# Optimization experiments

Measured on AMD Instinct MI355X. Metric: run time of the kernel, lower is better.

## Reference

```python
import jax, jax.numpy as jnp
import numpy as np

B, T, D_IN, H, D = 4, 4096, 1024, 16, 64


def setup_inputs() -> dict:
    key = jax.random.key(0)
    k1, k2, k3 = jax.random.split(key, 3)
    inputs = jax.random.normal(k1, (B, T, D_IN), dtype=jnp.float32)
    kv_kernel = jax.random.normal(k2, (D_IN, H, D, 2), dtype=jnp.float32) * (1.0 / np.sqrt(D_IN))
    q_kernel = jax.random.normal(k3, (H, D), dtype=jnp.float32) * (1.0 / np.sqrt(D))
    return {"inputs": inputs, "kv_kernel": kv_kernel, "q_kernel": q_kernel}


def _associate(a, b):
    # Online-softmax combine on packed tuples [m(1), u(1), w(D)] along last axis.
    ma, ua, wa = a[..., :1], a[..., 1:2], a[..., 2:]
    mb, ub, wb = b[..., :1], b[..., 1:2], b[..., 2:]
    m = jnp.maximum(ma, mb)
    ea = jnp.exp(ma - m)
    eb = jnp.exp(mb - m)
    u = ua * ea + ub * eb
    w = wa * ea + wb * eb
    return jnp.concatenate([m, u, w], axis=-1)


def reference(inputs, kv_kernel, q_kernel):
    # inputs: (B,T,D_in); kv_kernel: (D_in,H,D,2); q_kernel: (H,D)
    kv = jnp.einsum('bti,ihdk->bthdk', inputs, kv_kernel)
    kv = jax.nn.relu(kv)  # activation; dropout disabled (inference)
    k = kv[..., 0]  # (B,T,H,D)
    v = kv[..., 1]  # (B,T,H,D)
    st = jnp.einsum('hd,bthd->bth', q_kernel, k)[..., None]  # (B,T,H,1)
    u_init = jnp.ones_like(st)  # exp(s - m) with m = s
    elems = jnp.concatenate([st, u_init, v], axis=-1)  # (B,T,H,D+2)
    o = jax.lax.associative_scan(_associate, elems, axis=1)
    c = o[..., 1:2]  # running denominator
    a = o[..., 2:]   # running numerator (B,T,H,D)
    h = a / c
    # concat_heads=False -> sum over heads
    return jnp.sum(h, axis=-2)  # (B,T,D)
```

## Files before the change

kernel.cpp:

```cpp
#include <hip/hip_runtime.h>
#include <hip/hip_bf16.h>
#include <math.h>

#define B_   4
#define T_   4096
#define DIN_ 1024
#define H_   16
#define D_   64
#define M_   (B_*T_)
#define N_   (H_*D_*2)
#define K_   DIN_
#define C_   64
#define CL_  (T_/C_)

typedef unsigned short u16;
typedef __attribute__((ext_vector_type(8))) short short8_t;
typedef __attribute__((ext_vector_type(4))) float float4_t;

__device__ __forceinline__ u16 f2bf(float f) {
  unsigned int x = __float_as_uint(f);
  x += 0x7fffu + ((x >> 16) & 1u);
  return (u16)(x >> 16);
}
__device__ __forceinline__ float bf2f(unsigned int u) {
  return __uint_as_float((u & 0xffffu) << 16);
}
__device__ __forceinline__ unsigned pk_bf16(float x, float y) {
  float2 f; f.x = x; f.y = y;
  union { __hip_bfloat162 h2; unsigned u; } c;
  c.h2 = __float22bfloat162_rn(f);
  return c.u;
}

__device__ __forceinline__ void g2l16(const u16* g, u16* l) {
  __builtin_amdgcn_global_load_lds(
      (const __attribute__((address_space(1))) void*)g,
      (__attribute__((address_space(3))) void*)l, 16, 0, 0);
}

__global__ __launch_bounds__(256)
void prep(const float* __restrict__ inputs, const float* __restrict__ kvk,
          u16* __restrict__ aB, u16* __restrict__ wBt) {
  __shared__ float tile[32][33];
  int bid = blockIdx.x;
  int tid = threadIdx.x;
  if (bid < 8192) {
    int i = bid * 256 + tid;
    const float4* src = (const float4*)inputs;
    float4 a = src[2*i], b = src[2*i+1];
    uint4 o;
    o.x = pk_bf16(a.x, a.y);
    o.y = pk_bf16(a.z, a.w);
    o.z = pk_bf16(b.x, b.y);
    o.w = pk_bf16(b.z, b.w);
    ((uint4*)aB)[i] = o;
  } else {
    int b2 = bid - 8192;
    int kb = (b2 & 31) * 32;
    int nb = (b2 >> 5) * 32;
    int r  = tid >> 3;
    int c4 = (tid & 7) * 4;
    float4 v = *(const float4*)&kvk[(size_t)(kb + r) * N_ + nb + c4];
    tile[r][c4+0] = v.x; tile[r][c4+1] = v.y; tile[r][c4+2] = v.z; tile[r][c4+3] = v.w;
    __syncthreads();
    uint2 o;
    o.x = pk_bf16(tile[c4+0][r], tile[c4+1][r]);
    o.y = pk_bf16(tile[c4+2][r], tile[c4+3][r]);
    *(uint2*)&wBt[(size_t)(nb + r) * K_ + kb + c4] = o;
  }
}


#define FENCE asm volatile("" ::: "memory")
#define KBAR do { FENCE; __builtin_amdgcn_s_barrier(); FENCE; } while (0)

#define READS(PAR) do { _Pragma("unroll") \
  for (int i_ = 0; i_ < 4; ++i_) \
    af[i_] = *(const short8_t*)&lds[(PAR)*8192 + aBase + i_*512]; \
  _Pragma("unroll") \
  for (int j_ = 0; j_ < 4; ++j_) \
    bfq[j_] = *(const short8_t*)&lds[(PAR)*8192 + bBase + j_*512]; \
} while (0)

#define MFMAS do { \
  __builtin_amdgcn_s_setprio(1); \
  _Pragma("unroll") for (int i_ = 0; i_ < 4; ++i_) \
  _Pragma("unroll") for (int j_ = 0; j_ < 4; ++j_) \
    acc[i_][j_] = __builtin_amdgcn_mfma_f32_16x16x32_bf16( \
        af[i_], bfq[j_], acc[i_][j_], 0, 0, 0); \
  __builtin_amdgcn_s_setprio(0); \
} while (0)

#define PHASE(PAR, PAR2, KT) do { \
  short8_t af[4], bfq[4]; \
  READS(PAR); \
  g2l16(gA + ((KT)+2)*32, lds +         (PAR2)*8192 + wv*512); \
  g2l16(gB + ((KT)+2)*32, lds + 24576 + (PAR2)*8192 + wv*512); \
  KBAR; \
  MFMAS; \
  asm volatile("s_waitcnt vmcnt(2)" ::: "memory"); \
  KBAR; \
} while (0)

__global__ __launch_bounds__(1024)
void gemm_kv(const u16* __restrict__ A, const u16* __restrict__ Bt,
             const float* __restrict__ q,
             float* __restrict__ pbuf, u16* __restrict__ vbuf,
             float* __restrict__ aggU, float* __restrict__ aggW) {
  extern __shared__ __align__(16) char smem[];
  u16* lds = (u16*)smem;

  const int tid  = threadIdx.x;
  const int wv   = tid >> 6;
  const int lane = tid & 63;
  const int quad = lane >> 4;
  const int l16  = lane & 15;
  const int wr2  = wv >> 2;
  const int wc2  = wv & 3;

  const int g  = blockIdx.x;
  const int wg = (g & 7) * 64 + (g >> 3);
  const int nt = wg & 7;
  const int mt = wg >> 3;
  const int bm = mt * 256;
  const int bn = nt * 256;

  const u16* gA = A  + (size_t)(bm + (tid >> 2)) * K_ + (((tid & 3) ^ ((tid >> 3) & 3)) * 8);
  const u16* gB = Bt + (size_t)(bn + (tid >> 2)) * K_ + (((tid & 3) ^ ((tid >> 3) & 3)) * 8);

  const int sg    = (quad ^ ((l16 >> 1) & 3)) * 8;
  const int aBase = wr2 * 2048 + l16 * 32 + sg;
  const int bBase = 24576 + wc2 * 2048 + l16 * 32 + sg;

  float4_t acc[4][4] = {};

  g2l16(gA,      lds +                 wv*512);
  g2l16(gB,      lds + 24576 +         wv*512);
  g2l16(gA + 32, lds +          8192 + wv*512);
  g2l16(gB + 32, lds + 24576 +  8192 + wv*512);
  asm volatile("s_waitcnt vmcnt(2)" ::: "memory");
  KBAR;

#pragma unroll 1
  for (int kq = 0; kq < 10; ++kq) {
    const int kt = kq * 3;
    PHASE(0, 2, kt + 0);
    PHASE(1, 0, kt + 1);
    PHASE(2, 1, kt + 2);
  }
  {
    short8_t af[4], bfq[4];
    READS(0);
    KBAR;
    MFMAS;
    asm volatile("s_waitcnt vmcnt(0)" ::: "memory");
    KBAR;
  }
  {
    short8_t af[4], bfq[4];
    READS(1);
    KBAR;
    MFMAS;
    KBAR;
  }

  u16*   vtile = (u16*)smem;
  float* sred  = (float*)(smem + 73728);
  float* pS    = (float*)(smem + 83968);

  const int nh   = wc2 >> 1;
  const int wc2p = wc2 & 1;
  const int hd   = l16 >> 1;

  float qv[4];
#pragma unroll
  for (int j = 0; j < 4; ++j)
    qv[j] = q[(nt*2 + nh)*64 + wc2p*32 + j*8 + hd];

#pragma unroll
  for (int i = 0; i < 4; ++i) {
#pragma unroll
    for (int r = 0; r < 4; ++r) {
      const int t = wr2*64 + i*16 + quad*4 + r;
      float x0 = fmaxf(acc[i][0][r], 0.f);
      float x1 = fmaxf(acc[i][1][r], 0.f);
      float x2 = fmaxf(acc[i][2][r], 0.f);
      float x3 = fmaxf(acc[i][3][r], 0.f);
      if (l16 & 1) {
        vtile[(nh*256 + t)*72 + wc2p*32 +  0 + hd] = f2bf(x0);
        vtile[(nh*256 + t)*72 + wc2p*32 +  8 + hd] = f2bf(x1);
        vtile[(nh*256 + t)*72 + wc2p*32 + 16 + hd] = f2bf(x2);
        vtile[(nh*256 + t)*72 + wc2p*32 + 24 + hd] = f2bf(x3);
      } else {
        float ps = qv[0]*x0 + qv[1]*x1 + qv[2]*x2 + qv[3]*x3;
        ps += __shfl_xor(ps, 2);
        ps += __shfl_xor(ps, 4);
        if ((l16 & 7) == 0)
          sred[(nh*256 + t)*5 + wc2p*2 + (l16 >> 3)] = ps;
      }
    }
  }
  __syncthreads();

  const int b  = mt >> 4;
  const int t0 = (mt & 15) * 256;
  if (tid < 512) {
    const int hh = tid >> 8;
    const int t  = tid & 255;
    const float* sr = &sred[(hh*256 + t)*5];
    float s = sr[0] + sr[1] + sr[2] + sr[3];
    float p = __expf(fminf(fmaxf(s, -60.f), 60.f));
    pS[hh*256 + t] = p;
    pbuf[(size_t)(b*H_ + nt*2 + hh) * T_ + t0 + t] = p;
    float u = p;
#pragma unroll
    for (int off = 32; off; off >>= 1) u += __shfl_down(u, off);
    if (lane == 0)
      aggU[(b*H_ + nt*2 + hh)*C_ + (mt & 15)*4 + ((tid >> 6) & 3)] = u;
  }
  __syncthreads();

  if (l16 & 1) {
    float Wv[4] = {};
#pragma unroll
    for (int i = 0; i < 4; ++i)
#pragma unroll
      for (int r = 0; r < 4; ++r) {
        const int t = wr2*64 + i*16 + quad*4 + r;
        const float p = pS[nh*256 + t];
        Wv[0] += p * fmaxf(acc[i][0][r], 0.f);
        Wv[1] += p * fmaxf(acc[i][1][r], 0.f);
        Wv[2] += p * fmaxf(acc[i][2][r], 0.f);
        Wv[3] += p * fmaxf(acc[i][3][r], 0.f);
      }
#pragma unroll
    for (int j = 0; j < 4; ++j) {
      float w = Wv[j];
      w += __shfl_xor(w, 16);
      w += __shfl_xor(w, 32);
      if (quad == 0) {
        const int blk = (b*H_ + nt*2 + nh)*C_ + (mt & 15)*4 + wr2;
        aggW[(size_t)blk * D_ + wc2p*32 + j*8 + hd] = w;
      }
    }
  }
  {
    const int d0 = (tid & 7) * 8;
#pragma unroll
    for (int k2 = 0; k2 < 4; ++k2) {
      const int row = (tid >> 3) + 128*k2;
      const int hh  = row >> 8;
      const int t   = row & 255;
      uint4 val = *(const uint4*)&vtile[(hh*256 + t)*72 + d0];
      *(uint4*)&vbuf[((size_t)(b*H_ + nt*2 + hh) * T_ + t0 + t) * D_ + d0] = val;
    }
  }
}

__global__ __launch_bounds__(1024)
void scan_pass3(const u16* __restrict__ vbuf, const float* __restrict__ pbuf,
                const float* __restrict__ aggU, const float* __restrict__ aggW,
                float* __restrict__ out) {
  __shared__ float pS[H_][CL_];
  __shared__ float wbuf[H_][8][D_ + 1];
  int bc = blockIdx.x;
  int b  = bc >> 6;
  int c  = bc & (C_ - 1);
  int tid  = threadIdx.x;
  int h    = tid >> 6;
  int lane = tid & 63;
  int bh   = b * H_ + h;
  int t0   = c * CL_;

  pS[h][lane] = pbuf[(size_t)bh * T_ + t0 + lane];

  float U = 0.f, W = 0.f;
  for (int j = 0; j < c; ++j) {
    int idx = bh * C_ + j;
    U += aggU[idx];
    W += aggW[(size_t)idx * D_ + lane];
  }
  __syncthreads();

  const u16* vp = vbuf + ((size_t)bh * T_ + t0) * D_ + lane;
  for (int gg = 0; gg < 8; ++gg) {
#pragma unroll
    for (int ii = 0; ii < 8; ++ii) {
      int i = gg * 8 + ii;
      float p = pS[h][i];
      float v = bf2f(vp[i * D_]);
      U += p;
      W += p * v;
      wbuf[h][ii][lane] = __fdividef(W, U);
    }
    __syncthreads();
    if (tid < 512) {
      int ii = tid >> 6, dd = tid & 63;
      float acc = 0.f;
#pragma unroll
      for (int hh = 0; hh < H_; ++hh) acc += wbuf[hh][ii][dd];
      out[((size_t)b * T_ + t0 + gg*8 + ii) * D_ + dd] = acc;
    }
    __syncthreads();
  }
}

extern "C" void kernel_launch(void* const* d_in, const int* in_sizes, int n_in,
                              void* d_out, int out_size, void* d_ws, size_t ws_size,
                              hipStream_t stream) {
  const float* inputs = (const float*)d_in[0];
  const float* kvk    = (const float*)d_in[1];
  const float* qk     = (const float*)d_in[2];
  float* out = (float*)d_out;
  char* ws = (char*)d_ws;

  u16*   aB   = (u16*)ws;
  u16*   wBt  = (u16*)(ws + 33554432);
  u16*   vb   = (u16*)(ws + 37748736);
  float* pb   = (float*)(ws + 71303168);
  float* aggU = (float*)(ws + 72351744);
  float* aggW = (float*)(ws + 72368128);

  prep<<<10240, 256, 0, stream>>>(inputs, kvk, aB, wBt);
  gemm_kv<<<512, 1024, 98304, stream>>>(aB, wBt, qk, pb, vb, aggU, aggW);
  scan_pass3<<<B_*C_, 1024, 0, stream>>>(vb, pb, aggU, aggW, out);
}
```

Baseline: 202.5 us.

## Switch KV GEMM to 32x32x16 MFMA with 4-stage K16 pipeline and register double-buffering

Replaces the 16x16x32 MFMA tiling with 32x32x16 bf16 MFMAs. The K loop now uses a 4-deep LDS ring of K=16 slices, and fragment loads are double-buffered in registers so LDS reads overlap the MFMAs, with one barrier per step instead of two. The epilogue is remapped to the 32x32 accumulator layout. The prep kernel's conversion loads are split into two coalesced halves. This trades more barriers per K (64 smaller steps) and an unswizzled LDS layout (possible bank conflicts) for fewer instructions per FLOP and better overlap.

```diff
diff --git a/kernel.cpp b/kernel.cpp
--- a/kernel.cpp
+++ b/kernel.cpp
@@ -15,7 +15,7 @@
 
 typedef unsigned short u16;
 typedef __attribute__((ext_vector_type(8))) short short8_t;
-typedef __attribute__((ext_vector_type(4))) float float4_t;
+typedef __attribute__((ext_vector_type(16))) float f32x16;
 
 __device__ __forceinline__ u16 f2bf(float f) {
   unsigned int x = __float_as_uint(f);
@@ -45,15 +45,14 @@
   int bid = blockIdx.x;
   int tid = threadIdx.x;
   if (bid < 8192) {
-    int i = bid * 256 + tid;
-    const float4* src = (const float4*)inputs;
-    float4 a = src[2*i], b = src[2*i+1];
-    uint4 o;
-    o.x = pk_bf16(a.x, a.y);
-    o.y = pk_bf16(a.z, a.w);
-    o.z = pk_bf16(b.x, b.y);
-    o.w = pk_bf16(b.z, b.w);
-    ((uint4*)aB)[i] = o;
+    int j = bid * 256 + tid;
+    const float4* s4 = (const float4*)inputs;
+    float4 a = s4[j];
+    float4 b = s4[j + 2097152];
+    uint2 oa; oa.x = pk_bf16(a.x, a.y); oa.y = pk_bf16(a.z, a.w);
+    uint2 ob; ob.x = pk_bf16(b.x, b.y); ob.y = pk_bf16(b.z, b.w);
+    ((uint2*)aB)[j]           = oa;
+    ((uint2*)aB)[j + 2097152] = ob;
   } else {
     int b2 = bid - 8192;
     int kb = (b2 & 31) * 32;
@@ -74,31 +73,29 @@
 #define FENCE asm volatile("" ::: "memory")
 #define KBAR do { FENCE; __builtin_amdgcn_s_barrier(); FENCE; } while (0)
 
-#define READS(PAR) do { _Pragma("unroll") \
-  for (int i_ = 0; i_ < 4; ++i_) \
-    af[i_] = *(const short8_t*)&lds[(PAR)*8192 + aBase + i_*512]; \
-  _Pragma("unroll") \
-  for (int j_ = 0; j_ < 4; ++j_) \
-    bfq[j_] = *(const short8_t*)&lds[(PAR)*8192 + bBase + j_*512]; \
+#define MFMA32(a,b,c) __builtin_amdgcn_mfma_f32_32x32x16_bf16(a,b,c,0,0,0)
+
+#define LOADS(PN, AF, BF) do { \
+  AF[0] = *(const short8_t*)&lds[(PN)*4096 + aOff      ]; \
+  AF[1] = *(const short8_t*)&lds[(PN)*4096 + aOff + 512]; \
+  BF[0] = *(const short8_t*)&lds[16384 + (PN)*4096 + bOff      ]; \
+  BF[1] = *(const short8_t*)&lds[16384 + (PN)*4096 + bOff + 512]; \
 } while (0)
 
-#define MFMAS do { \
+#define MMAS(AF, BF) do { \
   __builtin_amdgcn_s_setprio(1); \
-  _Pragma("unroll") for (int i_ = 0; i_ < 4; ++i_) \
-  _Pragma("unroll") for (int j_ = 0; j_ < 4; ++j_) \
-    acc[i_][j_] = __builtin_amdgcn_mfma_f32_16x16x32_bf16( \
-        af[i_], bfq[j_], acc[i_][j_], 0, 0, 0); \
+  acc[0][0] = MFMA32(AF[0], BF[0], acc[0][0]); \
+  acc[0][1] = MFMA32(AF[0], BF[1], acc[0][1]); \
+  acc[1][0] = MFMA32(AF[1], BF[0], acc[1][0]); \
+  acc[1][1] = MFMA32(AF[1], BF[1], acc[1][1]); \
   __builtin_amdgcn_s_setprio(0); \
 } while (0)
 
-#define PHASE(PAR, PAR2, KT) do { \
-  short8_t af[4], bfq[4]; \
-  READS(PAR); \
-  g2l16(gA + ((KT)+2)*32, lds +         (PAR2)*8192 + wv*512); \
-  g2l16(gB + ((KT)+2)*32, lds + 24576 + (PAR2)*8192 + wv*512); \
-  KBAR; \
-  MFMAS; \
-  asm volatile("s_waitcnt vmcnt(2)" ::: "memory"); \
+#define PHASE(KT, PN, PS, AFm, BFm, AFl, BFl) do { \
+  LOADS(PN, AFl, BFl); \
+  g2l16(gS + (size_t)((KT)+3)*16, lds + stBase + (PS)*4096); \
+  MMAS(AFm, BFm); \
+  asm volatile("s_waitcnt vmcnt(1)" ::: "memory"); \
   KBAR; \
 } while (0)
 
@@ -113,8 +110,8 @@
   const int tid  = threadIdx.x;
   const int wv   = tid >> 6;
   const int lane = tid & 63;
-  const int quad = lane >> 4;
-  const int l16  = lane & 15;
+  const int l31  = lane & 31;
+  const int hi   = lane >> 5;
   const int wr2  = wv >> 2;
   const int wc2  = wv & 3;
 
@@ -125,78 +122,86 @@
   const int bm = mt * 256;
   const int bn = nt * 256;
 
-  const u16* gA = A  + (size_t)(bm + (tid >> 2)) * K_ + (((tid & 3) ^ ((tid >> 3) & 3)) * 8);
-  const u16* gB = Bt + (size_t)(bn + (tid >> 2)) * K_ + (((tid & 3) ^ ((tid >> 3) & 3)) * 8);
-
-  const int sg    = (quad ^ ((l16 >> 1) & 3)) * 8;
-  const int aBase = wr2 * 2048 + l16 * 32 + sg;
-  const int bBase = 24576 + wc2 * 2048 + l16 * 32 + sg;
-
-  float4_t acc[4][4] = {};
-
-  g2l16(gA,      lds +                 wv*512);
-  g2l16(gB,      lds + 24576 +         wv*512);
-  g2l16(gA + 32, lds +          8192 + wv*512);
-  g2l16(gB + 32, lds + 24576 +  8192 + wv*512);
-  asm volatile("s_waitcnt vmcnt(2)" ::: "memory");
+  const int stBase = (wv < 8) ? wv * 512 : 16384 + (wv - 8) * 512;
+  const u16* gS = (wv < 8)
+    ? A  + (size_t)(bm + wv*32       + (lane >> 1)) * K_ + (lane & 1) * 8
+    : Bt + (size_t)(bn + (wv-8)*32   + (lane >> 1)) * K_ + (lane & 1) * 8;
+
+  const int aOff = (wr2*64 + l31) * 16 + hi * 8;
+  const int bOff = (wc2*64 + l31) * 16 + hi * 8;
+
+  f32x16 acc[2][2] = {};
+  short8_t af0[2], bf0[2], af1[2], bf1[2];
+
+  g2l16(gS,      lds + stBase + 0*4096);
+  g2l16(gS + 16, lds + stBase + 1*4096);
+  g2l16(gS + 32, lds + stBase + 2*4096);
+  asm volatile("s_waitcnt vmcnt(1)" ::: "memory");
   KBAR;
+  LOADS(0, af0, bf0);
 
 #pragma unroll 1
-  for (int kq = 0; kq < 10; ++kq) {
-    const int kt = kq * 3;
-    PHASE(0, 2, kt + 0);
-    PHASE(1, 0, kt + 1);
-    PHASE(2, 1, kt + 2);
-  }
+  for (int kq = 0; kq < 7; ++kq) {
+    const int kt = kq * 8;
+    PHASE(kt+0, 1, 3, af0, bf0, af1, bf1);
+    PHASE(kt+1, 2, 0, af1, bf1, af0, bf0);
+    PHASE(kt+2, 3, 1, af0, bf0, af1, bf1);
+    PHASE(kt+3, 0, 2, af1, bf1, af0, bf0);
+    PHASE(kt+4, 1, 3, af0, bf0, af1, bf1);
+    PHASE(kt+5, 2, 0, af1, bf1, af0, bf0);
+    PHASE(kt+6, 3, 1, af0, bf0, af1, bf1);
+    PHASE(kt+7, 0, 2, af1, bf1, af0, bf0);
+  }
+  PHASE(56, 1, 3, af0, bf0, af1, bf1);
+  PHASE(57, 2, 0, af1, bf1, af0, bf0);
+  PHASE(58, 3, 1, af0, bf0, af1, bf1);
+  PHASE(59, 0, 2, af1, bf1, af0, bf0);
+  PHASE(60, 1, 3, af0, bf0, af1, bf1);
   {
-    short8_t af[4], bfq[4];
-    READS(0);
-    KBAR;
-    MFMAS;
+    LOADS(2, af0, bf0);
+    MMAS(af1, bf1);
     asm volatile("s_waitcnt vmcnt(0)" ::: "memory");
     KBAR;
   }
   {
-    short8_t af[4], bfq[4];
-    READS(1);
+    LOADS(3, af1, bf1);
+    MMAS(af0, bf0);
     KBAR;
-    MFMAS;
-    KBAR;
-  }
+  }
+  MMAS(af1, bf1);
 
   u16*   vtile = (u16*)smem;
   float* sred  = (float*)(smem + 73728);
   float* pS    = (float*)(smem + 83968);
 
+  __syncthreads();
+
   const int nh   = wc2 >> 1;
   const int wc2p = wc2 & 1;
-  const int hd   = l16 >> 1;
-
-  float qv[4];
-#pragma unroll
-  for (int j = 0; j < 4; ++j)
-    qv[j] = q[(nt*2 + nh)*64 + wc2p*32 + j*8 + hd];
-
-#pragma unroll
-  for (int i = 0; i < 4; ++i) {
-#pragma unroll
-    for (int r = 0; r < 4; ++r) {
-      const int t = wr2*64 + i*16 + quad*4 + r;
-      float x0 = fmaxf(acc[i][0][r], 0.f);
-      float x1 = fmaxf(acc[i][1][r], 0.f);
-      float x2 = fmaxf(acc[i][2][r], 0.f);
-      float x3 = fmaxf(acc[i][3][r], 0.f);
-      if (l16 & 1) {
-        vtile[(nh*256 + t)*72 + wc2p*32 +  0 + hd] = f2bf(x0);
-        vtile[(nh*256 + t)*72 + wc2p*32 +  8 + hd] = f2bf(x1);
-        vtile[(nh*256 + t)*72 + wc2p*32 + 16 + hd] = f2bf(x2);
-        vtile[(nh*256 + t)*72 + wc2p*32 + 24 + hd] = f2bf(x3);
+
+  float qv[2];
+  qv[0] = q[(nt*2 + nh)*64 + wc2p*32 +  0 + (l31 >> 1)];
+  qv[1] = q[(nt*2 + nh)*64 + wc2p*32 + 16 + (l31 >> 1)];
+
+#pragma unroll
+  for (int i = 0; i < 2; ++i) {
+#pragma unroll
+    for (int reg = 0; reg < 16; ++reg) {
+      const int t = wr2*64 + i*32 + (reg & 3) + 8*(reg >> 2) + 4*hi;
+      const float x0 = fmaxf(acc[i][0][reg], 0.f);
+      const float x1 = fmaxf(acc[i][1][reg], 0.f);
+      if (l31 & 1) {
+        const int d0 = wc2p*32 + (l31 >> 1);
+        vtile[(nh*256 + t)*72 + d0     ] = f2bf(x0);
+        vtile[(nh*256 + t)*72 + d0 + 16] = f2bf(x1);
       } else {
-        float ps = qv[0]*x0 + qv[1]*x1 + qv[2]*x2 + qv[3]*x3;
+        float ps = qv[0]*x0 + qv[1]*x1;
         ps += __shfl_xor(ps, 2);
         ps += __shfl_xor(ps, 4);
-        if ((l16 & 7) == 0)
-          sred[(nh*256 + t)*5 + wc2p*2 + (l16 >> 3)] = ps;
+        ps += __shfl_xor(ps, 8);
+        ps += __shfl_xor(ps, 16);
+        if (l31 == 0)
+          sred[(nh*256 + t)*5 + wc2p] = ps;
       }
     }
   }
@@ -208,7 +213,7 @@
     const int hh = tid >> 8;
     const int t  = tid & 255;
     const float* sr = &sred[(hh*256 + t)*5];
-    float s = sr[0] + sr[1] + sr[2] + sr[3];
+    float s = sr[0] + sr[1];
     float p = __expf(fminf(fmaxf(s, -60.f), 60.f));
     pS[hh*256 + t] = p;
     pbuf[(size_t)(b*H_ + nt*2 + hh) * T_ + t0 + t] = p;
@@ -220,28 +225,23 @@
   }
   __syncthreads();
 
-  if (l16 & 1) {
-    float Wv[4] = {};
-#pragma unroll
-    for (int i = 0; i < 4; ++i)
-#pragma unroll
-      for (int r = 0; r < 4; ++r) {
-        const int t = wr2*64 + i*16 + quad*4 + r;
+  if (l31 & 1) {
+    float Wv0 = 0.f, Wv1 = 0.f;
+#pragma unroll
+    for (int i = 0; i < 2; ++i)
+#pragma unroll
+      for (int reg = 0; reg < 16; ++reg) {
+        const int t = wr2*64 + i*32 + (reg & 3) + 8*(reg >> 2) + 4*hi;
         const float p = pS[nh*256 + t];
-        Wv[0] += p * fmaxf(acc[i][0][r], 0.f);
-        Wv[1] += p * fmaxf(acc[i][1][r], 0.f);
-        Wv[2] += p * fmaxf(acc[i][2][r], 0.f);
-        Wv[3] += p * fmaxf(acc[i][3][r], 0.f);
+        Wv0 += p * fmaxf(acc[i][0][reg], 0.f);
+        Wv1 += p * fmaxf(acc[i][1][reg], 0.f);
       }
-#pragma unroll
-    for (int j = 0; j < 4; ++j) {
-      float w = Wv[j];
-      w += __shfl_xor(w, 16);
-      w += __shfl_xor(w, 32);
-      if (quad == 0) {
-        const int blk = (b*H_ + nt*2 + nh)*C_ + (mt & 15)*4 + wr2;
-        aggW[(size_t)blk * D_ + wc2p*32 + j*8 + hd] = w;
-      }
+    Wv0 += __shfl_xor(Wv0, 32);
+    Wv1 += __shfl_xor(Wv1, 32);
+    if (hi == 0) {
+      const int blk = (b*H_ + nt*2 + nh)*C_ + (mt & 15)*4 + wr2;
+      aggW[(size_t)blk * D_ + wc2p*32 +  0 + (l31 >> 1)] = Wv0;
+      aggW[(size_t)blk * D_ + wc2p*32 + 16 + (l31 >> 1)] = Wv1;
     }
   }
   {
@@ -322,6 +322,6 @@
   float* aggW = (float*)(ws + 72368128);
 
   prep<<<10240, 256, 0, stream>>>(inputs, kvk, aB, wBt);
-  gemm_kv<<<512, 1024, 98304, stream>>>(aB, wBt, qk, pb, vb, aggU, aggW);
+  gemm_kv<<<512, 1024, 86016, stream>>>(aB, wBt, qk, pb, vb, aggU, aggW);
   scan_pass3<<<B_*C_, 1024, 0, stream>>>(vb, pb, aggU, aggW, out);
 }
```

After: 236.6 us. +16.8%, slower.
